# Performance work log

Hardware: AMD Instinct MI355X
Metric: run time of the kernel (lower is better)

The kernel has to match this reference:

```python
import jax, jax.numpy as jnp
import numpy as np

NUM_LAYERS = 2
D_MODEL = 64
D_INNER = 128   # expand * d_model
D_STATE = 128   # min(2*input_size, 256)
DT_RANK = 4     # ceil(d_model / 16)
D_CONV = 4
HIDDEN = 64


def _causal_dwconv(x, w, b):
    # x: [B, L, C], w: [C, K], b: [C]  -- causal depthwise conv (left pad K-1)
    K = w.shape[1]
    L = x.shape[1]
    xp = jnp.pad(x, ((0, 0), (K - 1, 0), (0, 0)))
    y = sum(xp[:, k:k + L, :] * w[:, k][None, None, :] for k in range(K))
    return y + b


def _selective_scan(u, delta, A, B, C, Dp):
    # u, delta: [b,L,d]; A: [d,n]; B, C: [b,L,n]; Dp: [d]
    dA = jnp.exp(jnp.einsum('bld,dn->lbdn', delta, A))          # [L,b,d,n]
    dBu = jnp.einsum('bld,bln,bld->lbdn', delta, B, u)           # [L,b,d,n]
    Ct = jnp.swapaxes(C, 0, 1)                                   # [L,b,n]

    def step(h, inp):
        dA_t, dBu_t, C_t = inp
        h = dA_t * h + dBu_t                                     # [b,d,n]
        y = jnp.einsum('bdn,bn->bd', h, C_t)
        return h, y

    h0 = jnp.zeros(dA.shape[1:], dA.dtype)
    _, ys = jax.lax.scan(step, h0, (dA, dBu, Ct))                # ys: [L,b,d]
    return jnp.swapaxes(ys, 0, 1) + u * Dp


def _mamba_layer(x, in_w, conv_w, conv_b, xproj_w, dt_w, dt_b, A_log, Dp, out_w):
    xz = x @ in_w.T                                              # [B,L,2*d_inner]
    xi, z = jnp.split(xz, 2, axis=-1)
    xi = jax.nn.silu(_causal_dwconv(xi, conv_w, conv_b))
    xdbl = xi @ xproj_w.T                                        # [B,L,dt_rank+2*d_state]
    delta = jax.nn.softplus(xdbl[..., :DT_RANK] @ dt_w.T + dt_b)
    Bm = xdbl[..., DT_RANK:DT_RANK + D_STATE]
    Cm = xdbl[..., DT_RANK + D_STATE:]
    A = -jnp.exp(A_log)
    y = _selective_scan(xi, delta, A, Bm, Cm, Dp)
    y = y * jax.nn.silu(z)
    return y @ out_w.T


def setup_inputs() -> dict:
    key = jax.random.key(0)
    ks = jax.random.split(key, 10)
    B, L = 4, 1024
    s = 0.05
    x = jax.random.normal(ks[0], (B, L, D_MODEL), dtype=jnp.float32)
    in_proj_w = jax.random.normal(ks[1], (NUM_LAYERS, 2 * D_INNER, D_MODEL)) * s
    conv_w = jax.random.normal(ks[2], (NUM_LAYERS, D_INNER, D_CONV)) * 0.2
    conv_b = jax.random.normal(ks[3], (NUM_LAYERS, D_INNER)) * 0.02
    x_proj_w = jax.random.normal(ks[4], (NUM_LAYERS, DT_RANK + 2 * D_STATE, D_INNER)) * s
    dt_w = jax.random.normal(ks[5], (NUM_LAYERS, D_INNER, DT_RANK)) * 0.1
    dt_b = jnp.full((NUM_LAYERS, D_INNER), -4.6, dtype=jnp.float32)  # softplus -> ~0.01
    # S4D-real init: A_log = log(1..d_state)
    A_log = jnp.log(jnp.broadcast_to(
        jnp.arange(1, D_STATE + 1, dtype=jnp.float32), (NUM_LAYERS, D_INNER, D_STATE)))
    D = jnp.ones((NUM_LAYERS, D_INNER), dtype=jnp.float32)
    out_proj_w = jax.random.normal(ks[6], (NUM_LAYERS, D_MODEL, D_INNER)) * s
    fc_w = jax.random.normal(ks[7], (HIDDEN, D_MODEL)) * s
    fc_b = jax.random.normal(ks[8], (HIDDEN,)) * 0.02
    return {"x": x, "in_proj_w": in_proj_w, "conv_w": conv_w, "conv_b": conv_b,
            "x_proj_w": x_proj_w, "dt_w": dt_w, "dt_b": dt_b, "A_log": A_log,
            "D": D, "out_proj_w": out_proj_w, "fc_w": fc_w, "fc_b": fc_b}


def reference(x, in_proj_w, conv_w, conv_b, x_proj_w, dt_w, dt_b, A_log, D, out_proj_w, fc_w, fc_b):
    h = x
    for l in range(NUM_LAYERS):
        h = _mamba_layer(h, in_proj_w[l], conv_w[l], conv_b[l], x_proj_w[l],
                         dt_w[l], dt_b[l], A_log[l], D[l], out_proj_w[l])
    return h @ fc_w.T + fc_b
```

## Files before the change

### kernel.cpp

```cpp
#include <hip/hip_runtime.h>
#include <hip/hip_bf16.h>
#include <hip/hip_cooperative_groups.h>

namespace cg = cooperative_groups;

#define BB 4
#define LL 1024
#define DM 64
#define DI 128
#define DS 128
#define DTR 4
#define KC 4
#define RT 8
#define GRP 8
#define CS 64
#define NC 16
#define L2E 1.44269504f

#define XWT_OFF   0
#define INWT_OFF  65536
#define OWT_OFF   98304
#define CWT_OFF   114688
#define CB_OFF    115712
#define DTWT_OFF  115968
#define DTB_OFF   116992
#define XWDT_OFF  117248

__device__ __forceinline__ float bf2f(__hip_bfloat16 v) { return __bfloat162float(v); }
__device__ __forceinline__ float silu_f(float x) { return x / (1.f + __expf(-x)); }

__device__ __forceinline__ float ldf(const void* p, long i, unsigned bf) {
    return bf ? __bfloat162float(((const __hip_bfloat16*)p)[i]) : ((const float*)p)[i];
}

__device__ __forceinline__ void fma4(float4& acc, float s, const float4 w) {
    acc.x = fmaf(s, w.x, acc.x); acc.y = fmaf(s, w.y, acc.y);
    acc.z = fmaf(s, w.z, acc.z); acc.w = fmaf(s, w.w, acc.w);
}

__device__ __forceinline__ void probe_flags(const void* dtb, const void* fcw,
                                            unsigned& bfe, unsigned& bfw) {
    unsigned w = *(const unsigned*)dtb;
    bfe = (w == 0xC093C093u) ? 1u : 0u;
    const unsigned* p = (const unsigned*)fcw;
    int cnt = 0;
    for (int i = 0; i < 32; ++i) {
        unsigned m = p[i] & 0x7FFFu;
        if (m >= 0x3000u && m < 0x4200u) cnt++;
    }
    bfw = (cnt >= 28) ? 1u : 0u;
}

__global__ __launch_bounds__(256) void k_prep(
        const void* __restrict__ inw, const void* __restrict__ xw,
        const void* __restrict__ ow, const void* __restrict__ cw,
        const void* __restrict__ cb, const void* __restrict__ dtw,
        const void* __restrict__ dtb, const void* __restrict__ fcw,
        unsigned* __restrict__ flags, float* __restrict__ WT) {
    unsigned bfe, bfw;
    probe_flags(dtb, fcw, bfe, bfw);
    int bid = blockIdx.x, tid = threadIdx.x;
    if (bid < 28) {
        const void* src; long soff; int srcK; float* dst; int dstN; int n0, k0;
        if (bid < 16) {
            int l = bid >> 3, kt = (bid >> 2) & 1, nt = bid & 3;
            src = xw; srcK = 128; soff = (long)l * 260 * 128 + 4 * 128;
            n0 = nt * 64; k0 = kt * 64; dst = WT + XWT_OFF + l * 32768; dstN = 256;
        } else if (bid < 24) {
            int b2 = bid - 16, l = b2 >> 2, nt = b2 & 3;
            src = inw; srcK = 64; soff = (long)l * 256 * 64;
            n0 = nt * 64; k0 = 0; dst = WT + INWT_OFF + l * 16384; dstN = 256;
        } else {
            int b2 = bid - 24, l = b2 >> 1, kt = b2 & 1;
            src = ow; srcK = 128; soff = (long)l * 64 * 128;
            n0 = 0; k0 = kt * 64; dst = WT + OWT_OFF + l * 8192; dstN = 64;
        }
        __shared__ float tile[64 * 65];
        for (int i = tid; i < 4096; i += 256) {
            int ln = i >> 6, lk = i & 63;
            tile[ln * 65 + lk] = ldf(src, soff + (long)(n0 + ln) * srcK + k0 + lk, bfw);
        }
        __syncthreads();
        for (int i = tid; i < 4096; i += 256) {
            int lk = i >> 6, ln = i & 63;
            dst[(long)(k0 + lk) * dstN + n0 + ln] = tile[ln * 65 + lk];
        }
    } else {
        if (tid == 0) { flags[0] = bfe; flags[1] = bfw; flags[2] = bfe & bfw; }
        for (int j = tid; j < 1024; j += 256) {
            int l = j >> 9, t = (j >> 7) & 3, d = j & 127;
            WT[CWT_OFF + j] = ldf(cw, (long)l * 512 + d * 4 + t, bfw);
        }
        for (int j = tid; j < 256; j += 256) WT[CB_OFF + j] = ldf(cb, j, bfw);
        for (int j = tid; j < 1024; j += 256) {
            int l = j >> 9, r = (j >> 7) & 3, d = j & 127;
            WT[DTWT_OFF + j] = ldf(dtw, (long)l * 512 + d * 4 + r, bfw);
        }
        for (int j = tid; j < 256; j += 256) WT[DTB_OFF + j] = ldf(dtb, j, bfe);
        for (int j = tid; j < 1024; j += 256) {
            int l = j >> 9, rem = j & 511;
            WT[XWDT_OFF + j] = ldf(xw, (long)l * 260 * 128 + rem, bfw);
        }
    }
}

__global__ __launch_bounds__(256) void k_inproj(
        const void* __restrict__ xin, int xin_probe,
        const float* __restrict__ wt, const unsigned* __restrict__ flags,
        float* __restrict__ xzx, float* __restrict__ sz) {
    unsigned bfx = xin_probe ? flags[0] : 0u;
    int row0 = blockIdx.x * RT;
    int tid = threadIdx.x, lane = tid & 63, g = tid >> 6;
    __shared__ float act[RT * DM];
    for (int i = tid; i < RT * DM; i += 256)
        act[i] = ldf(xin, (long)(row0 + (i >> 6)) * DM + (i & 63), bfx);
    __syncthreads();
    const float4* wt4 = (const float4*)wt;
    float4 acc[2];
    acc[0] = make_float4(0.f, 0.f, 0.f, 0.f);
    acc[1] = make_float4(0.f, 0.f, 0.f, 0.f);
#pragma unroll 8
    for (int k4 = 0; k4 < DM / 4; ++k4) {
        float4 w0 = wt4[(k4 * 4 + 0) * 64 + lane];
        float4 w1 = wt4[(k4 * 4 + 1) * 64 + lane];
        float4 w2 = wt4[(k4 * 4 + 2) * 64 + lane];
        float4 w3 = wt4[(k4 * 4 + 3) * 64 + lane];
#pragma unroll
        for (int r = 0; r < 2; ++r) {
            float4 av = *(const float4*)&act[(g * 2 + r) * DM + k4 * 4];
            fma4(acc[r], av.x, w0); fma4(acc[r], av.y, w1);
            fma4(acc[r], av.z, w2); fma4(acc[r], av.w, w3);
        }
    }
    int n0 = lane * 4;
#pragma unroll
    for (int r = 0; r < 2; ++r) {
        int row = row0 + g * 2 + r;
        if (n0 < DI) {
            *(float4*)&xzx[(size_t)row * DI + n0] = acc[r];
        } else {
            float4 v;
            v.x = silu_f(acc[r].x); v.y = silu_f(acc[r].y);
            v.z = silu_f(acc[r].z); v.w = silu_f(acc[r].w);
            *(float4*)&sz[(size_t)row * DI + (n0 - DI)] = v;
        }
    }
}

__global__ __launch_bounds__(256) void k_xproj(
        const float* __restrict__ xzx,
        const float* __restrict__ cwT, const float* __restrict__ cbF,
        const float* __restrict__ xwT, const float* __restrict__ xwdtF,
        const float* __restrict__ dtwT, const float* __restrict__ dtbF,
        float* __restrict__ xiw, float* __restrict__ dlt,
        float* __restrict__ Bm, float* __restrict__ Cm) {
    int row0 = blockIdx.x * RT;
    int b = row0 >> 10, l0 = row0 & (LL - 1);
    int tid = threadIdx.x, lane = tid & 63, g = tid >> 6;
    __shared__ float xc[(RT + KC - 1) * DI];
    __shared__ float act[RT * DI];
    __shared__ float dtp[RT * DTR];
    for (int i = tid; i < (RT + KC - 1) * DI; i += 256) {
        int r = (i >> 7) - (KC - 1);
        int l = l0 + r;
        xc[i] = (l >= 0) ? xzx[((size_t)b * LL + l) * DI + (i & 127)] : 0.f;
    }
    __syncthreads();
    for (int i = tid; i < RT * DI; i += 256) {
        int r = i >> 7, d = i & 127;
        float a = cbF[d];
#pragma unroll
        for (int t = 0; t < KC; ++t) a = fmaf(xc[(r + t) * DI + d], cwT[t * DI + d], a);
        float v = silu_f(a);
        act[i] = v;
        xiw[(size_t)(row0 + r) * DI + d] = v;
    }
    __syncthreads();
    const float4* wt4 = (const float4*)xwT;
    float4 acc[2];
    acc[0] = make_float4(0.f, 0.f, 0.f, 0.f);
    acc[1] = make_float4(0.f, 0.f, 0.f, 0.f);
#pragma unroll 8
    for (int k4 = 0; k4 < DI / 4; ++k4) {
        float4 w0 = wt4[(k4 * 4 + 0) * 64 + lane];
        float4 w1 = wt4[(k4 * 4 + 1) * 64 + lane];
        float4 w2 = wt4[(k4 * 4 + 2) * 64 + lane];
        float4 w3 = wt4[(k4 * 4 + 3) * 64 + lane];
#pragma unroll
        for (int r = 0; r < 2; ++r) {
            float4 av = *(const float4*)&act[(g * 2 + r) * DI + k4 * 4];
            fma4(acc[r], av.x, w0); fma4(acc[r], av.y, w1);
            fma4(acc[r], av.z, w2); fma4(acc[r], av.w, w3);
        }
    }
    int n0 = lane * 4;
#pragma unroll
    for (int r = 0; r < 2; ++r) {
        int row = row0 + g * 2 + r;
        if (n0 < DS) *(float4*)&Bm[(size_t)row * DS + n0] = acc[r];
        else         *(float4*)&Cm[(size_t)row * DS + (n0 - DS)] = acc[r];
    }
    if (tid < RT * DTR) {
        int r = tid >> 2, i = tid & 3;
        float a = 0.f;
#pragma unroll
        for (int k4 = 0; k4 < DI / 4; ++k4) {
            float4 av = *(const float4*)&act[r * DI + k4 * 4];
            float4 wv = *(const float4*)&xwdtF[i * DI + k4 * 4];
            a = fmaf(av.x, wv.x, a); a = fmaf(av.y, wv.y, a);
            a = fmaf(av.z, wv.z, a); a = fmaf(av.w, wv.w, a);
        }
        dtp[tid] = a;
    }
    __syncthreads();
    if (tid < DI) {
        float dw0 = dtwT[0 * DI + tid], dw1 = dtwT[1 * DI + tid];
        float dw2 = dtwT[2 * DI + tid], dw3 = dtwT[3 * DI + tid];
        float bv = dtbF[tid];
#pragma unroll
        for (int r = 0; r < RT; ++r) {
            float a = bv;
            a = fmaf(dtp[r * 4 + 0], dw0, a);
            a = fmaf(dtp[r * 4 + 1], dw1, a);
            a = fmaf(dtp[r * 4 + 2], dw2, a);
            a = fmaf(dtp[r * 4 + 3], dw3, a);
            dlt[(size_t)(row0 + r) * DI + tid] = (a > 20.f) ? a : log1pf(__expf(a));
        }
    }
}

__global__ __launch_bounds__(256) void k_scanF(
        const float* __restrict__ dlt, const float* __restrict__ xiw,
        const float* __restrict__ Bm, const float* __restrict__ Cm,
        const void* __restrict__ Alog, long aoff,
        const void* __restrict__ Dp, long doff,
        const unsigned* __restrict__ flags,
        float* __restrict__ hend, float* __restrict__ S,
        float* __restrict__ y) {
    __shared__ float dsh[CS * 4];
    __shared__ float dush[CS * 4];
    __shared__ float cdsh[CS * 4];
    __shared__ float ysh[CS * 4];
    __shared__ float Wred[4 * 520];
    int gid = blockIdx.x;
    int dg = gid / (BB * NC);
    int bc = gid % (BB * NC);
    int b = bc / NC, c = bc % NC;
    int d0 = dg * 4;
    int tid = threadIdx.x;
    int w = tid >> 6, t = tid & 63;
    int d = d0 + w;
    int c0 = c * CS;
    unsigned bfe = flags[0];
    float A0 = -L2E * __expf(ldf(Alog, aoff + (long)d * DS + 2 * t, bfe));
    float A1 = -L2E * __expf(ldf(Alog, aoff + (long)d * DS + 2 * t + 1, bfe));
    for (int i = tid; i < CS * 4; i += 256) {
        size_t src = ((size_t)b * LL + c0 + (i >> 2)) * DI + d0 + (i & 3);
        float dl = dlt[src];
        float ul = xiw[src];
        dsh[i] = dl;
        dush[i] = dl * ul;
        ysh[i] = ul * ldf(Dp, doff + d0 + (i & 3), bfe);
    }
    __syncthreads();
    {
        float a = dsh[t * 4 + w];
#pragma unroll
        for (int off = 1; off < 64; off <<= 1) {
            float n = __shfl(a, t - off, 64);
            if (t >= off) a += n;
        }
        cdsh[t * 4 + w] = a;
    }
    const float2* Bg = (const float2*)(Bm + ((size_t)b * LL + c0) * DS) + t;
    const float2* Cg = (const float2*)(Cm + ((size_t)b * LL + c0) * DS) + t;
    float* Wl = Wred + w * 520;
    int rbase = (t >> 3) * 65 + (t & 7) * 8;
    float h0 = 0.f, h1v = 0.f;
    for (int li = 0; li < CS; li += GRP) {
        float dl[GRP], du[GRP], ea0[GRP], ea1[GRP], cv[GRP];
        float2 Bv[GRP], Cv[GRP];
#pragma unroll
        for (int s = 0; s < GRP; ++s) {
            dl[s] = dsh[(li + s) * 4 + w];
            du[s] = dush[(li + s) * 4 + w];
            Bv[s] = Bg[(size_t)(li + s) * (DS / 2)];
            Cv[s] = Cg[(size_t)(li + s) * (DS / 2)];
        }
#pragma unroll
        for (int s = 0; s < GRP; ++s) {
            ea0[s] = exp2f(dl[s] * A0);
            ea1[s] = exp2f(dl[s] * A1);
        }
#pragma unroll
        for (int s = 0; s < GRP; ++s) {
            h0  = fmaf(ea0[s], h0,  du[s] * Bv[s].x);
            h1v = fmaf(ea1[s], h1v, du[s] * Bv[s].y);
            cv[s] = fmaf(h0, Cv[s].x, h1v * Cv[s].y);
        }
#pragma unroll
        for (int s = 0; s < GRP; ++s) Wl[s * 65 + t] = cv[s];
        float pt = 0.f;
#pragma unroll
        for (int j = 0; j < 8; ++j) pt += Wl[rbase + j];
        pt += __shfl_xor(pt, 1, 64);
        pt += __shfl_xor(pt, 2, 64);
        pt += __shfl_xor(pt, 4, 64);
        if ((t & 7) == 0) {
            int l = li + (t >> 3);
            ysh[l * 4 + w] += pt;
        }
    }
    if (c < NC - 1) {
        size_t hbase = (((size_t)b * DI + d) * NC + c) * DS;
        ((float2*)(hend + hbase))[t] = make_float2(h0, h1v);
        if (t == 0) S[((size_t)b * DI + d) * NC + c] = cdsh[(CS - 1) * 4 + w];
    }
    __threadfence();
    cg::this_grid().sync();
    if (c > 0) {
        float hi0 = 0.f, hi1 = 0.f, ssum = 0.f;
        const float2* hep = (const float2*)(hend + (((size_t)b * DI + d) * NC) * DS);
        const float* Sp = S + ((size_t)b * DI + d) * NC;
        for (int cc = c - 1; cc >= 0; --cc) {
            float2 he = hep[(size_t)cc * (DS / 2) + t];
            hi0 = fmaf(exp2f(A0 * ssum), he.x, hi0);
            hi1 = fmaf(exp2f(A1 * ssum), he.y, hi1);
            ssum += Sp[cc];
        }
        for (int li = 0; li < CS; li += GRP) {
            float cd[GRP], ea0[GRP], ea1[GRP], cv[GRP];
            float2 Cv[GRP];
#pragma unroll
            for (int s = 0; s < GRP; ++s) {
                cd[s] = cdsh[(li + s) * 4 + w];
                Cv[s] = Cg[(size_t)(li + s) * (DS / 2)];
            }
#pragma unroll
            for (int s = 0; s < GRP; ++s) {
                ea0[s] = exp2f(cd[s] * A0);
                ea1[s] = exp2f(cd[s] * A1);
            }
#pragma unroll
            for (int s = 0; s < GRP; ++s)
                cv[s] = fmaf(hi0 * ea0[s], Cv[s].x, hi1 * ea1[s] * Cv[s].y);
#pragma unroll
            for (int s = 0; s < GRP; ++s) Wl[s * 65 + t] = cv[s];
            float pt = 0.f;
#pragma unroll
            for (int j = 0; j < 8; ++j) pt += Wl[rbase + j];
            pt += __shfl_xor(pt, 1, 64);
            pt += __shfl_xor(pt, 2, 64);
            pt += __shfl_xor(pt, 4, 64);
            if ((t & 7) == 0) {
                int l = li + (t >> 3);
                ysh[l * 4 + w] += pt;
            }
        }
    }
    __syncthreads();
    for (int i = tid; i < CS * 4; i += 256)
        y[((size_t)b * LL + c0 + (i >> 2)) * DI + d0 + (i & 3)] = ysh[i];
}

__global__ __launch_bounds__(256) void k_scanA(
        const float* __restrict__ dlt, const float* __restrict__ xiw,
        const float* __restrict__ Bm,
        const void* __restrict__ Alog, long aoff,
        const unsigned* __restrict__ flags,
        float* __restrict__ hend, float* __restrict__ S) {
    __shared__ float dsh[CS * 4];
    __shared__ float ush[CS * 4];
    int gid = blockIdx.x;
    int dg = gid / (BB * NC);
    int bc = gid % (BB * NC);
    int b = bc / NC, c = bc % NC;
    int d0 = dg * 4;
    int tid = threadIdx.x;
    int w = tid >> 6, t = tid & 63;
    int d = d0 + w;
    int c0 = c * CS;
    unsigned bfe = flags[0];
    float A0 = -L2E * __expf(ldf(Alog, aoff + (long)d * DS + 2 * t, bfe));
    float A1 = -L2E * __expf(ldf(Alog, aoff + (long)d * DS + 2 * t + 1, bfe));
    for (int i = tid; i < CS * 4; i += 256) {
        size_t src = ((size_t)b * LL + c0 + (i >> 2)) * DI + d0 + (i & 3);
        dsh[i] = dlt[src];
        ush[i] = xiw[src];
    }
    __syncthreads();
    const float2* Bg = (const float2*)(Bm + ((size_t)b * LL + c0) * DS) + t;
    float h0 = 0.f, h1v = 0.f, sumd = 0.f;
    for (int li = 0; li < CS; li += GRP) {
        float dl[GRP], ul[GRP], ea0[GRP], ea1[GRP];
        float2 Bv[GRP];
#pragma unroll
        for (int s = 0; s < GRP; ++s) {
            dl[s] = dsh[(li + s) * 4 + w];
            ul[s] = ush[(li + s) * 4 + w];
            Bv[s] = Bg[(size_t)(li + s) * (DS / 2)];
        }
#pragma unroll
        for (int s = 0; s < GRP; ++s) {
            ea0[s] = exp2f(dl[s] * A0);
            ea1[s] = exp2f(dl[s] * A1);
        }
#pragma unroll
        for (int s = 0; s < GRP; ++s) {
            float db = dl[s] * ul[s];
            h0  = fmaf(ea0[s], h0,  db * Bv[s].x);
            h1v = fmaf(ea1[s], h1v, db * Bv[s].y);
            sumd += dl[s];
        }
    }
    size_t hbase = (((size_t)b * DI + d) * NC + c) * DS;
    ((float2*)(hend + hbase))[t] = make_float2(h0, h1v);
    if (t == 0) S[((size_t)b * DI + d) * NC + c] = sumd;
}

__global__ __launch_bounds__(256) void k_scanC(
        const float* __restrict__ dlt, const float* __restrict__ xiw,
        const float* __restrict__ Bm, const float* __restrict__ Cm,
        const void* __restrict__ Alog, long aoff,
        const void* __restrict__ Dp, long doff,
        const unsigned* __restrict__ flags,
        const float* __restrict__ hend, const float* __restrict__ S,
        float* __restrict__ y) {
    __shared__ float dsh[CS * 4];
    __shared__ float ush[CS * 4];
    __shared__ float ysh[CS * 4];
    __shared__ float Wred[4 * 520];
    int gid = blockIdx.x;
    int dg = gid / (BB * NC);
    int bc = gid % (BB * NC);
    int b = bc / NC, c = bc % NC;
    int d0 = dg * 4;
    int tid = threadIdx.x;
    int w = tid >> 6, t = tid & 63;
    int d = d0 + w;
    int c0 = c * CS;
    unsigned bfe = flags[0];
    float A0 = -L2E * __expf(ldf(Alog, aoff + (long)d * DS + 2 * t, bfe));
    float A1 = -L2E * __expf(ldf(Alog, aoff + (long)d * DS + 2 * t + 1, bfe));
    float Dv = ldf(Dp, doff + d, bfe);
    for (int i = tid; i < CS * 4; i += 256) {
        size_t src = ((size_t)b * LL + c0 + (i >> 2)) * DI + d0 + (i & 3);
        dsh[i] = dlt[src];
        ush[i] = xiw[src];
    }
    __syncthreads();
    float h0 = 0.f, h1v = 0.f, ssum = 0.f;
    const float2* hep = (const float2*)(hend + (((size_t)b * DI + d) * NC) * DS);
    const float* Sp = S + ((size_t)b * DI + d) * NC;
    for (int cc = c - 1; cc >= 0; --cc) {
        float2 he = hep[(size_t)cc * (DS / 2) + t];
        h0  = fmaf(exp2f(A0 * ssum), he.x, h0);
        h1v = fmaf(exp2f(A1 * ssum), he.y, h1v);
        ssum += Sp[cc];
    }
    const float2* Bg = (const float2*)(Bm + ((size_t)b * LL + c0) * DS) + t;
    const float2* Cg = (const float2*)(Cm + ((size_t)b * LL + c0) * DS) + t;
    float* Wl = Wred + w * 520;
    int rbase = (t >> 3) * 65 + (t & 7) * 8;
    for (int li = 0; li < CS; li += GRP) {
        float dl[GRP], ul[GRP], ea0[GRP], ea1[GRP], cv[GRP];
        float2 Bv[GRP], Cv[GRP];
#pragma unroll
        for (int s = 0; s < GRP; ++s) {
            dl[s] = dsh[(li + s) * 4 + w];
            ul[s] = ush[(li + s) * 4 + w];
            Bv[s] = Bg[(size_t)(li + s) * (DS / 2)];
            Cv[s] = Cg[(size_t)(li + s) * (DS / 2)];
        }
#pragma unroll
        for (int s = 0; s < GRP; ++s) {
            ea0[s] = exp2f(dl[s] * A0);
            ea1[s] = exp2f(dl[s] * A1);
        }
#pragma unroll
        for (int s = 0; s < GRP; ++s) {
            float db = dl[s] * ul[s];
            h0  = fmaf(ea0[s], h0,  db * Bv[s].x);
            h1v = fmaf(ea1[s], h1v, db * Bv[s].y);
            cv[s] = fmaf(h0, Cv[s].x, h1v * Cv[s].y);
        }
#pragma unroll
        for (int s = 0; s < GRP; ++s) Wl[s * 65 + t] = cv[s];
        float pt = 0.f;
#pragma unroll
        for (int j = 0; j < 8; ++j) pt += Wl[rbase + j];
        pt += __shfl_xor(pt, 1, 64);
        pt += __shfl_xor(pt, 2, 64);
        pt += __shfl_xor(pt, 4, 64);
        if ((t & 7) == 0) {
            int l = li + (t >> 3);
            ysh[l * 4 + w] = pt + ush[l * 4 + w] * Dv;
        }
    }
    __syncthreads();
    for (int i = tid; i < CS * 4; i += 256)
        y[((size_t)b * LL + c0 + (i >> 2)) * DI + d0 + (i & 3)] = ysh[i];
}

__global__ __launch_bounds__(256) void k_out(
        const float* __restrict__ y, const float* __restrict__ sz,
        const float* __restrict__ owT, float* __restrict__ hout) {
    int row0 = blockIdx.x * RT;
    int tid = threadIdx.x, n = tid & 63, g = tid >> 6;
    __shared__ float act[RT * DI];
    for (int i = tid; i < RT * DI; i += 256) {
        size_t idx = (size_t)(row0 + (i >> 7)) * DI + (i & 127);
        act[i] = y[idx] * sz[idx];
    }
    __syncthreads();
    float acc[2] = {0.f, 0.f};
#pragma unroll 8
    for (int k4 = 0; k4 < DI / 4; ++k4) {
        float w0 = owT[(k4 * 4 + 0) * DM + n];
        float w1 = owT[(k4 * 4 + 1) * DM + n];
        float w2 = owT[(k4 * 4 + 2) * DM + n];
        float w3 = owT[(k4 * 4 + 3) * DM + n];
#pragma unroll
        for (int r = 0; r < 2; ++r) {
            float4 av = *(const float4*)&act[(g * 2 + r) * DI + k4 * 4];
            acc[r] = fmaf(av.x, w0, acc[r]); acc[r] = fmaf(av.y, w1, acc[r]);
            acc[r] = fmaf(av.z, w2, acc[r]); acc[r] = fmaf(av.w, w3, acc[r]);
        }
    }
#pragma unroll
    for (int r = 0; r < 2; ++r)
        hout[(size_t)(row0 + g * 2 + r) * DM + n] = acc[r];
}

__global__ __launch_bounds__(256) void k_fc(
        const float* __restrict__ h, const void* __restrict__ fw,
        const void* __restrict__ fb, const unsigned* __restrict__ flags,
        void* __restrict__ out) {
    unsigned bfw = flags[1], obf = flags[2];
    int row0 = blockIdx.x * RT;
    int tid = threadIdx.x, n = tid & 63, g = tid >> 6;
    __shared__ float wsh[DM * 65];
    __shared__ float act[RT * DM];
    for (int i = tid; i < DM * DM; i += 256) {
        int nn = i >> 6, k = i & 63;
        wsh[k * 65 + nn] = ldf(fw, i, bfw);
    }
    for (int i = tid; i < RT * DM; i += 256)
        act[i] = h[(size_t)(row0 + (i >> 6)) * DM + (i & 63)];
    __syncthreads();
    float bv = ldf(fb, n, bfw);
    float acc[2] = {bv, bv};
#pragma unroll 8
    for (int k4 = 0; k4 < DM / 4; ++k4) {
        float w0 = wsh[(k4 * 4 + 0) * 65 + n];
        float w1 = wsh[(k4 * 4 + 1) * 65 + n];
        float w2 = wsh[(k4 * 4 + 2) * 65 + n];
        float w3 = wsh[(k4 * 4 + 3) * 65 + n];
#pragma unroll
        for (int r = 0; r < 2; ++r) {
            float4 av = *(const float4*)&act[(g * 2 + r) * DM + k4 * 4];
            acc[r] = fmaf(av.x, w0, acc[r]); acc[r] = fmaf(av.y, w1, acc[r]);
            acc[r] = fmaf(av.z, w2, acc[r]); acc[r] = fmaf(av.w, w3, acc[r]);
        }
    }
#pragma unroll
    for (int r = 0; r < 2; ++r) {
        size_t idx = (size_t)(row0 + g * 2 + r) * DM + n;
        if (obf) ((__hip_bfloat16*)out)[idx] = __float2bfloat16(acc[r]);
        else     ((float*)out)[idx] = acc[r];
    }
}

extern "C" void kernel_launch(void* const* d_in, const int* in_sizes, int n_in,
                              void* d_out, int out_size, void* d_ws, size_t ws_size,
                              hipStream_t stream) {
    const void* x    = d_in[0];
    const void* inw  = d_in[1];
    const void* cw   = d_in[2];
    const void* cb   = d_in[3];
    const void* xw   = d_in[4];
    const void* dtw  = d_in[5];
    const void* dtb  = d_in[6];
    const void* Alog = d_in[7];
    const void* Dp   = d_in[8];
    const void* ow   = d_in[9];
    const void* fcw  = d_in[10];
    const void* fcb  = d_in[11];

    const size_t NBL = (size_t)BB * LL;
    const int GB = (int)(NBL / RT);
    unsigned* flags = (unsigned*)d_ws;
    float* base = (float*)d_ws + 64;
    float* h1   = base;
    float* sz   = h1 + 262144;
    float* xiw  = sz + 524288;
    float* dlt  = xiw + 524288;
    float* Bmw  = dlt + 524288;
    float* Cmw  = Bmw + 524288;
    float* yw   = Cmw + 524288;
    float* hend = yw + 524288;
    float* S    = hend + 1048576;
    float* xzx  = yw;
    float* WT   = (float*)d_out;

    int nb = 0;
    hipOccupancyMaxActiveBlocksPerMultiprocessor(&nb, k_scanF, 256, 0);
    const bool coop = (nb >= 8);

    k_prep<<<29, 256, 0, stream>>>(inw, xw, ow, cw, cb, dtw, dtb, fcw, flags, WT);

    for (int l = 0; l < 2; ++l) {
        const void* xin = (l == 0) ? x : (const void*)h1;
        int xmode = (l == 0) ? 1 : 0;
        k_inproj<<<GB, 256, 0, stream>>>(xin, xmode, WT + INWT_OFF + l * 16384, flags, xzx, sz);
        k_xproj<<<GB, 256, 0, stream>>>(xzx,
                                        WT + CWT_OFF + l * 512, WT + CB_OFF + l * 128,
                                        WT + XWT_OFF + l * 32768, WT + XWDT_OFF + l * 512,
                                        WT + DTWT_OFF + l * 512, WT + DTB_OFF + l * 128,
                                        xiw, dlt, Bmw, Cmw);
        long ao = (long)l * DI * DS;
        long dof = (long)l * DI;
        if (coop) {
            const float* dlt_c = dlt; const float* xiw_c = xiw;
            const float* Bm_c = Bmw; const float* Cm_c = Cmw;
            const unsigned* fl_c = flags;
            void* params[] = {
                (void*)&dlt_c, (void*)&xiw_c, (void*)&Bm_c, (void*)&Cm_c,
                (void*)&Alog, (void*)&ao, (void*)&Dp, (void*)&dof,
                (void*)&fl_c, (void*)&hend, (void*)&S, (void*)&yw
            };
            hipLaunchCooperativeKernel((const void*)k_scanF, dim3(32 * BB * NC),
                                       dim3(256), params, 0, stream);
        } else {
            k_scanA<<<32 * BB * NC, 256, 0, stream>>>(dlt, xiw, Bmw, Alog, ao, flags, hend, S);
            k_scanC<<<32 * BB * NC, 256, 0, stream>>>(dlt, xiw, Bmw, Cmw, Alog, ao,
                                                      Dp, dof, flags, hend, S, yw);
        }
        k_out<<<GB, 256, 0, stream>>>(yw, sz, WT + OWT_OFF + l * 8192, h1);
    }
    k_fc<<<GB, 256, 0, stream>>>(h1, fcw, fcb, flags, d_out);
}
```

Before: 299.0 us.

## Replace chunked cooperative scan with sequential full-length scan per channel pair

Removes the chunk-parallel scan, which ran a local pass, a grid-wide sync and a carry-propagation pass, and replaces it with a plain sequential scan over all 1024 steps. Each block handles two channels for one batch, with one state element per thread, and B/C loads are double-buffered in registers. The D*u skip term moves into the output projection kernel. This drops the grid sync, the extra pass and the hend/S traffic, at the cost of a long serial dependency chain and only 256 blocks.

```diff
diff --git a/kernel.cpp b/kernel.cpp
--- a/kernel.cpp
+++ b/kernel.cpp
@@ -1,8 +1,5 @@
 #include <hip/hip_runtime.h>
 #include <hip/hip_bf16.h>
-#include <hip/hip_cooperative_groups.h>
-
-namespace cg = cooperative_groups;
 
 #define BB 4
 #define LL 1024
@@ -12,9 +9,7 @@
 #define DTR 4
 #define KC 4
 #define RT 8
-#define GRP 8
-#define CS 64
-#define NC 16
+#define SGRP 8
 #define L2E 1.44269504f
 
 #define XWT_OFF   0
@@ -26,7 +21,6 @@
 #define DTB_OFF   116992
 #define XWDT_OFF  117248
 
-__device__ __forceinline__ float bf2f(__hip_bfloat16 v) { return __bfloat162float(v); }
 __device__ __forceinline__ float silu_f(float x) { return x / (1.f + __expf(-x)); }
 
 __device__ __forceinline__ float ldf(const void* p, long i, unsigned bf) {
@@ -229,288 +223,104 @@
     }
 }
 
-__global__ __launch_bounds__(256) void k_scanF(
+#define SCAN_GROUP(LI, BV, CV)                                              \
+    {                                                                       \
+        float dl0[SGRP], du0[SGRP], ea[SGRP], cv[SGRP];                     \
+        _Pragma("unroll") for (int s = 0; s < SGRP; ++s) {                  \
+            dl0[s] = dsh[d_loc][(LI) + s];                                  \
+            du0[s] = dush[d_loc][(LI) + s];                                 \
+        }                                                                   \
+        _Pragma("unroll") for (int s = 0; s < SGRP; ++s)                    \
+            ea[s] = exp2f(dl0[s] * A);                                      \
+        _Pragma("unroll") for (int s = 0; s < SGRP; ++s) {                  \
+            h = fmaf(ea[s], h, du0[s] * BV[s]);                             \
+            cv[s] = h * CV[s];                                              \
+        }                                                                   \
+        _Pragma("unroll") for (int s = 0; s < SGRP; ++s)                    \
+            Wl[s * 65 + t] = cv[s];                                         \
+        float pt = 0.f;                                                     \
+        _Pragma("unroll") for (int j = 0; j < 8; ++j) pt += Wl[rbase + j];  \
+        pt += __shfl_xor(pt, 1, 64);                                        \
+        pt += __shfl_xor(pt, 2, 64);                                        \
+        pt += __shfl_xor(pt, 4, 64);                                        \
+        if ((t & 7) == 0) ysh[((LI) + (t >> 3)) * 4 + w] = pt;              \
+    }
+
+__global__ __launch_bounds__(256) void k_scan(
         const float* __restrict__ dlt, const float* __restrict__ xiw,
         const float* __restrict__ Bm, const float* __restrict__ Cm,
         const void* __restrict__ Alog, long aoff,
+        const unsigned* __restrict__ flags,
+        float* __restrict__ y) {
+    __shared__ float dsh[2][LL];
+    __shared__ float dush[2][LL];
+    __shared__ float ysh[LL * 4];
+    __shared__ float Wred[4 * 520];
+    int bid = blockIdx.x;
+    int b = bid >> 6, dg = bid & 63;
+    int tid = threadIdx.x, w = tid >> 6, t = tid & 63;
+    int d_loc = w >> 1, half = w & 1;
+    int d = dg * 2 + d_loc;
+    int n = half * 64 + t;
+    unsigned bfe = flags[0];
+    float A = -L2E * __expf(ldf(Alog, aoff + (long)d * DS + n, bfe));
+    for (int i = tid; i < 2 * LL; i += 256) {
+        int l = i >> 1, dd = i & 1;
+        size_t src = ((size_t)b * LL + l) * DI + dg * 2 + dd;
+        float dl = dlt[src];
+        dsh[dd][l] = dl;
+        dush[dd][l] = dl * xiw[src];
+    }
+    __syncthreads();
+    const float* Bg = Bm + (size_t)b * LL * DS + n;
+    const float* Cg = Cm + (size_t)b * LL * DS + n;
+    float* Wl = Wred + w * 520;
+    int rbase = (t >> 3) * 65 + (t & 7) * 8;
+    float h = 0.f;
+    float B0[SGRP], C0[SGRP], B1[SGRP], C1[SGRP];
+#pragma unroll
+    for (int s = 0; s < SGRP; ++s) {
+        B0[s] = Bg[(size_t)s * DS];
+        C0[s] = Cg[(size_t)s * DS];
+    }
+    for (int li = 0; li < LL; li += 2 * SGRP) {
+#pragma unroll
+        for (int s = 0; s < SGRP; ++s) {
+            B1[s] = Bg[(size_t)(li + SGRP + s) * DS];
+            C1[s] = Cg[(size_t)(li + SGRP + s) * DS];
+        }
+        SCAN_GROUP(li, B0, C0);
+#pragma unroll
+        for (int s = 0; s < SGRP; ++s) {
+            B0[s] = Bg[(size_t)(li + 2 * SGRP + s) * DS];
+            C0[s] = Cg[(size_t)(li + 2 * SGRP + s) * DS];
+        }
+        SCAN_GROUP(li + SGRP, B1, C1);
+    }
+    __syncthreads();
+    for (int i = tid; i < LL * 2; i += 256) {
+        int l = i >> 1, dd = i & 1;
+        y[((size_t)b * LL + l) * DI + dg * 2 + dd] =
+            ysh[l * 4 + dd * 2] + ysh[l * 4 + dd * 2 + 1];
+    }
+}
+
+__global__ __launch_bounds__(256) void k_out(
+        const float* __restrict__ y, const float* __restrict__ sz,
+        const float* __restrict__ xiw,
         const void* __restrict__ Dp, long doff,
         const unsigned* __restrict__ flags,
-        float* __restrict__ hend, float* __restrict__ S,
-        float* __restrict__ y) {
-    __shared__ float dsh[CS * 4];
-    __shared__ float dush[CS * 4];
-    __shared__ float cdsh[CS * 4];
-    __shared__ float ysh[CS * 4];
-    __shared__ float Wred[4 * 520];
-    int gid = blockIdx.x;
-    int dg = gid / (BB * NC);
-    int bc = gid % (BB * NC);
-    int b = bc / NC, c = bc % NC;
-    int d0 = dg * 4;
-    int tid = threadIdx.x;
-    int w = tid >> 6, t = tid & 63;
-    int d = d0 + w;
-    int c0 = c * CS;
+        const float* __restrict__ owT, float* __restrict__ hout) {
     unsigned bfe = flags[0];
-    float A0 = -L2E * __expf(ldf(Alog, aoff + (long)d * DS + 2 * t, bfe));
-    float A1 = -L2E * __expf(ldf(Alog, aoff + (long)d * DS + 2 * t + 1, bfe));
-    for (int i = tid; i < CS * 4; i += 256) {
-        size_t src = ((size_t)b * LL + c0 + (i >> 2)) * DI + d0 + (i & 3);
-        float dl = dlt[src];
-        float ul = xiw[src];
-        dsh[i] = dl;
-        dush[i] = dl * ul;
-        ysh[i] = ul * ldf(Dp, doff + d0 + (i & 3), bfe);
-    }
-    __syncthreads();
-    {
-        float a = dsh[t * 4 + w];
-#pragma unroll
-        for (int off = 1; off < 64; off <<= 1) {
-            float n = __shfl(a, t - off, 64);
-            if (t >= off) a += n;
-        }
-        cdsh[t * 4 + w] = a;
-    }
-    const float2* Bg = (const float2*)(Bm + ((size_t)b * LL + c0) * DS) + t;
-    const float2* Cg = (const float2*)(Cm + ((size_t)b * LL + c0) * DS) + t;
-    float* Wl = Wred + w * 520;
-    int rbase = (t >> 3) * 65 + (t & 7) * 8;
-    float h0 = 0.f, h1v = 0.f;
-    for (int li = 0; li < CS; li += GRP) {
-        float dl[GRP], du[GRP], ea0[GRP], ea1[GRP], cv[GRP];
-        float2 Bv[GRP], Cv[GRP];
-#pragma unroll
-        for (int s = 0; s < GRP; ++s) {
-            dl[s] = dsh[(li + s) * 4 + w];
-            du[s] = dush[(li + s) * 4 + w];
-            Bv[s] = Bg[(size_t)(li + s) * (DS / 2)];
-            Cv[s] = Cg[(size_t)(li + s) * (DS / 2)];
-        }
-#pragma unroll
-        for (int s = 0; s < GRP; ++s) {
-            ea0[s] = exp2f(dl[s] * A0);
-            ea1[s] = exp2f(dl[s] * A1);
-        }
-#pragma unroll
-        for (int s = 0; s < GRP; ++s) {
-            h0  = fmaf(ea0[s], h0,  du[s] * Bv[s].x);
-            h1v = fmaf(ea1[s], h1v, du[s] * Bv[s].y);
-            cv[s] = fmaf(h0, Cv[s].x, h1v * Cv[s].y);
-        }
-#pragma unroll
-        for (int s = 0; s < GRP; ++s) Wl[s * 65 + t] = cv[s];
-        float pt = 0.f;
-#pragma unroll
-        for (int j = 0; j < 8; ++j) pt += Wl[rbase + j];
-        pt += __shfl_xor(pt, 1, 64);
-        pt += __shfl_xor(pt, 2, 64);
-        pt += __shfl_xor(pt, 4, 64);
-        if ((t & 7) == 0) {
-            int l = li + (t >> 3);
-            ysh[l * 4 + w] += pt;
-        }
-    }
-    if (c < NC - 1) {
-        size_t hbase = (((size_t)b * DI + d) * NC + c) * DS;
-        ((float2*)(hend + hbase))[t] = make_float2(h0, h1v);
-        if (t == 0) S[((size_t)b * DI + d) * NC + c] = cdsh[(CS - 1) * 4 + w];
-    }
-    __threadfence();
-    cg::this_grid().sync();
-    if (c > 0) {
-        float hi0 = 0.f, hi1 = 0.f, ssum = 0.f;
-        const float2* hep = (const float2*)(hend + (((size_t)b * DI + d) * NC) * DS);
-        const float* Sp = S + ((size_t)b * DI + d) * NC;
-        for (int cc = c - 1; cc >= 0; --cc) {
-            float2 he = hep[(size_t)cc * (DS / 2) + t];
-            hi0 = fmaf(exp2f(A0 * ssum), he.x, hi0);
-            hi1 = fmaf(exp2f(A1 * ssum), he.y, hi1);
-            ssum += Sp[cc];
-        }
-        for (int li = 0; li < CS; li += GRP) {
-            float cd[GRP], ea0[GRP], ea1[GRP], cv[GRP];
-            float2 Cv[GRP];
-#pragma unroll
-            for (int s = 0; s < GRP; ++s) {
-                cd[s] = cdsh[(li + s) * 4 + w];
-                Cv[s] = Cg[(size_t)(li + s) * (DS / 2)];
-            }
-#pragma unroll
-            for (int s = 0; s < GRP; ++s) {
-                ea0[s] = exp2f(cd[s] * A0);
-                ea1[s] = exp2f(cd[s] * A1);
-            }
-#pragma unroll
-            for (int s = 0; s < GRP; ++s)
-                cv[s] = fmaf(hi0 * ea0[s], Cv[s].x, hi1 * ea1[s] * Cv[s].y);
-#pragma unroll
-            for (int s = 0; s < GRP; ++s) Wl[s * 65 + t] = cv[s];
-            float pt = 0.f;
-#pragma unroll
-            for (int j = 0; j < 8; ++j) pt += Wl[rbase + j];
-            pt += __shfl_xor(pt, 1, 64);
-            pt += __shfl_xor(pt, 2, 64);
-            pt += __shfl_xor(pt, 4, 64);
-            if ((t & 7) == 0) {
-                int l = li + (t >> 3);
-                ysh[l * 4 + w] += pt;
-            }
-        }
-    }
-    __syncthreads();
-    for (int i = tid; i < CS * 4; i += 256)
-        y[((size_t)b * LL + c0 + (i >> 2)) * DI + d0 + (i & 3)] = ysh[i];
-}
-
-__global__ __launch_bounds__(256) void k_scanA(
-        const float* __restrict__ dlt, const float* __restrict__ xiw,
-        const float* __restrict__ Bm,
-        const void* __restrict__ Alog, long aoff,
-        const unsigned* __restrict__ flags,
-        float* __restrict__ hend, float* __restrict__ S) {
-    __shared__ float dsh[CS * 4];
-    __shared__ float ush[CS * 4];
-    int gid = blockIdx.x;
-    int dg = gid / (BB * NC);
-    int bc = gid % (BB * NC);
-    int b = bc / NC, c = bc % NC;
-    int d0 = dg * 4;
-    int tid = threadIdx.x;
-    int w = tid >> 6, t = tid & 63;
-    int d = d0 + w;
-    int c0 = c * CS;
-    unsigned bfe = flags[0];
-    float A0 = -L2E * __expf(ldf(Alog, aoff + (long)d * DS + 2 * t, bfe));
-    float A1 = -L2E * __expf(ldf(Alog, aoff + (long)d * DS + 2 * t + 1, bfe));
-    for (int i = tid; i < CS * 4; i += 256) {
-        size_t src = ((size_t)b * LL + c0 + (i >> 2)) * DI + d0 + (i & 3);
-        dsh[i] = dlt[src];
-        ush[i] = xiw[src];
-    }
-    __syncthreads();
-    const float2* Bg = (const float2*)(Bm + ((size_t)b * LL + c0) * DS) + t;
-    float h0 = 0.f, h1v = 0.f, sumd = 0.f;
-    for (int li = 0; li < CS; li += GRP) {
-        float dl[GRP], ul[GRP], ea0[GRP], ea1[GRP];
-        float2 Bv[GRP];
-#pragma unroll
-        for (int s = 0; s < GRP; ++s) {
-            dl[s] = dsh[(li + s) * 4 + w];
-            ul[s] = ush[(li + s) * 4 + w];
-            Bv[s] = Bg[(size_t)(li + s) * (DS / 2)];
-        }
-#pragma unroll
-        for (int s = 0; s < GRP; ++s) {
-            ea0[s] = exp2f(dl[s] * A0);
-            ea1[s] = exp2f(dl[s] * A1);
-        }
-#pragma unroll
-        for (int s = 0; s < GRP; ++s) {
-            float db = dl[s] * ul[s];
-            h0  = fmaf(ea0[s], h0,  db * Bv[s].x);
-            h1v = fmaf(ea1[s], h1v, db * Bv[s].y);
-            sumd += dl[s];
-        }
-    }
-    size_t hbase = (((size_t)b * DI + d) * NC + c) * DS;
-    ((float2*)(hend + hbase))[t] = make_float2(h0, h1v);
-    if (t == 0) S[((size_t)b * DI + d) * NC + c] = sumd;
-}
-
-__global__ __launch_bounds__(256) void k_scanC(
-        const float* __restrict__ dlt, const float* __restrict__ xiw,
-        const float* __restrict__ Bm, const float* __restrict__ Cm,
-        const void* __restrict__ Alog, long aoff,
-        const void* __restrict__ Dp, long doff,
-        const unsigned* __restrict__ flags,
-        const float* __restrict__ hend, const float* __restrict__ S,
-        float* __restrict__ y) {
-    __shared__ float dsh[CS * 4];
-    __shared__ float ush[CS * 4];
-    __shared__ float ysh[CS * 4];
-    __shared__ float Wred[4 * 520];
-    int gid = blockIdx.x;
-    int dg = gid / (BB * NC);
-    int bc = gid % (BB * NC);
-    int b = bc / NC, c = bc % NC;
-    int d0 = dg * 4;
-    int tid = threadIdx.x;
-    int w = tid >> 6, t = tid & 63;
-    int d = d0 + w;
-    int c0 = c * CS;
-    unsigned bfe = flags[0];
-    float A0 = -L2E * __expf(ldf(Alog, aoff + (long)d * DS + 2 * t, bfe));
-    float A1 = -L2E * __expf(ldf(Alog, aoff + (long)d * DS + 2 * t + 1, bfe));
-    float Dv = ldf(Dp, doff + d, bfe);
-    for (int i = tid; i < CS * 4; i += 256) {
-        size_t src = ((size_t)b * LL + c0 + (i >> 2)) * DI + d0 + (i & 3);
-        dsh[i] = dlt[src];
-        ush[i] = xiw[src];
-    }
-    __syncthreads();
-    float h0 = 0.f, h1v = 0.f, ssum = 0.f;
-    const float2* hep = (const float2*)(hend + (((size_t)b * DI + d) * NC) * DS);
-    const float* Sp = S + ((size_t)b * DI + d) * NC;
-    for (int cc = c - 1; cc >= 0; --cc) {
-        float2 he = hep[(size_t)cc * (DS / 2) + t];
-        h0  = fmaf(exp2f(A0 * ssum), he.x, h0);
-        h1v = fmaf(exp2f(A1 * ssum), he.y, h1v);
-        ssum += Sp[cc];
-    }
-    const float2* Bg = (const float2*)(Bm + ((size_t)b * LL + c0) * DS) + t;
-    const float2* Cg = (const float2*)(Cm + ((size_t)b * LL + c0) * DS) + t;
-    float* Wl = Wred + w * 520;
-    int rbase = (t >> 3) * 65 + (t & 7) * 8;
-    for (int li = 0; li < CS; li += GRP) {
-        float dl[GRP], ul[GRP], ea0[GRP], ea1[GRP], cv[GRP];
-        float2 Bv[GRP], Cv[GRP];
-#pragma unroll
-        for (int s = 0; s < GRP; ++s) {
-            dl[s] = dsh[(li + s) * 4 + w];
-            ul[s] = ush[(li + s) * 4 + w];
-            Bv[s] = Bg[(size_t)(li + s) * (DS / 2)];
-            Cv[s] = Cg[(size_t)(li + s) * (DS / 2)];
-        }
-#pragma unroll
-        for (int s = 0; s < GRP; ++s) {
-            ea0[s] = exp2f(dl[s] * A0);
-            ea1[s] = exp2f(dl[s] * A1);
-        }
-#pragma unroll
-        for (int s = 0; s < GRP; ++s) {
-            float db = dl[s] * ul[s];
-            h0  = fmaf(ea0[s], h0,  db * Bv[s].x);
-            h1v = fmaf(ea1[s], h1v, db * Bv[s].y);
-            cv[s] = fmaf(h0, Cv[s].x, h1v * Cv[s].y);
-        }
-#pragma unroll
-        for (int s = 0; s < GRP; ++s) Wl[s * 65 + t] = cv[s];
-        float pt = 0.f;
-#pragma unroll
-        for (int j = 0; j < 8; ++j) pt += Wl[rbase + j];
-        pt += __shfl_xor(pt, 1, 64);
-        pt += __shfl_xor(pt, 2, 64);
-        pt += __shfl_xor(pt, 4, 64);
-        if ((t & 7) == 0) {
-            int l = li + (t >> 3);
-            ysh[l * 4 + w] = pt + ush[l * 4 + w] * Dv;
-        }
-    }
-    __syncthreads();
-    for (int i = tid; i < CS * 4; i += 256)
-        y[((size_t)b * LL + c0 + (i >> 2)) * DI + d0 + (i & 3)] = ysh[i];
-}
-
-__global__ __launch_bounds__(256) void k_out(
-        const float* __restrict__ y, const float* __restrict__ sz,
-        const float* __restrict__ owT, float* __restrict__ hout) {
     int row0 = blockIdx.x * RT;
     int tid = threadIdx.x, n = tid & 63, g = tid >> 6;
     __shared__ float act[RT * DI];
+    __shared__ float Dsh[DI];
+    if (tid < DI) Dsh[tid] = ldf(Dp, doff + tid, bfe);
+    __syncthreads();
     for (int i = tid; i < RT * DI; i += 256) {
         size_t idx = (size_t)(row0 + (i >> 7)) * DI + (i & 127);
-        act[i] = y[idx] * sz[idx];
+        act[i] = (y[idx] + xiw[idx] * Dsh[i & 127]) * sz[idx];
     }
     __syncthreads();
     float acc[2] = {0.f, 0.f};
@@ -598,14 +408,8 @@
     float* Bmw  = dlt + 524288;
     float* Cmw  = Bmw + 524288;
     float* yw   = Cmw + 524288;
-    float* hend = yw + 524288;
-    float* S    = hend + 1048576;
     float* xzx  = yw;
     float* WT   = (float*)d_out;
-
-    int nb = 0;
-    hipOccupancyMaxActiveBlocksPerMultiprocessor(&nb, k_scanF, 256, 0);
-    const bool coop = (nb >= 8);
 
     k_prep<<<29, 256, 0, stream>>>(inw, xw, ow, cw, cb, dtw, dtb, fcw, flags, WT);
 
@@ -620,23 +424,9 @@
                                         xiw, dlt, Bmw, Cmw);
         long ao = (long)l * DI * DS;
         long dof = (long)l * DI;
-        if (coop) {
-            const float* dlt_c = dlt; const float* xiw_c = xiw;
-            const float* Bm_c = Bmw; const float* Cm_c = Cmw;
-            const unsigned* fl_c = flags;
-            void* params[] = {
-                (void*)&dlt_c, (void*)&xiw_c, (void*)&Bm_c, (void*)&Cm_c,
-                (void*)&Alog, (void*)&ao, (void*)&Dp, (void*)&dof,
-                (void*)&fl_c, (void*)&hend, (void*)&S, (void*)&yw
-            };
-            hipLaunchCooperativeKernel((const void*)k_scanF, dim3(32 * BB * NC),
-                                       dim3(256), params, 0, stream);
-        } else {
-            k_scanA<<<32 * BB * NC, 256, 0, stream>>>(dlt, xiw, Bmw, Alog, ao, flags, hend, S);
-            k_scanC<<<32 * BB * NC, 256, 0, stream>>>(dlt, xiw, Bmw, Cmw, Alog, ao,
-                                                      Dp, dof, flags, hend, S, yw);
-        }
-        k_out<<<GB, 256, 0, stream>>>(yw, sz, WT + OWT_OFF + l * 8192, h1);
+        k_scan<<<BB * 64, 256, 0, stream>>>(dlt, xiw, Bmw, Cmw, Alog, ao, flags, yw);
+        k_out<<<GB, 256, 0, stream>>>(yw, sz, xiw, Dp, dof, flags,
+                                      WT + OWT_OFF + l * 8192, h1);
     }
     k_fc<<<GB, 256, 0, stream>>>(h1, fcw, fcb, flags, d_out);
 }
```

Measured after the change: 317.4 us. 6.1% more time.
